# Performance work log

Hardware: AMD Instinct MI355X
Metric: run time of the kernel (lower is better)

The kernel has to match this reference:

```python
import jax, jax.numpy as jnp
import numpy as np

BETA = 0.25
DECAY = 0.99
USAGE_DECAY = 0.99
EPS = 1e-5
RESET_THRESHOLD = 100.0


def _sqdist(x, e):
    # squared euclidean distances [N, K]; argmin identical to cdist argmin
    x2 = jnp.sum(x * x, axis=1, keepdims=True)           # [N,1]
    e2 = jnp.sum(e * e, axis=1)[None, :]                 # [1,K]
    return x2 - 2.0 * (x @ e.T) + e2


def setup_inputs() -> dict:
    key = jax.random.key(0)
    ks = jax.random.split(key, 7)
    N, K, D = 32768, 4096, 256
    return {
        "x": jax.random.normal(ks[0], (N, D), jnp.float32),
        "embedding": jax.random.normal(ks[1], (K, D), jnp.float32) * (1.0 / K),
        "ema_cluster_size": jax.random.uniform(ks[2], (K,), jnp.float32),
        "ema_w": jax.random.normal(ks[3], (K, D), jnp.float32) * (1.0 / K),
        "codebook_usage": jax.random.uniform(ks[4], (K,), jnp.float32),
        "steps_since_used": jax.random.randint(ks[5], (K,), 0, 200, jnp.int32),
        "random_indices": jax.random.randint(ks[6], (K,), 0, N, jnp.int32),
    }


def reference(x, embedding, ema_cluster_size, ema_w, codebook_usage,
              steps_since_used, random_indices):
    N, D = x.shape
    K = embedding.shape[0]

    # --- nearest-code lookup ---
    d2 = _sqdist(x, embedding)                 # [N,K]
    indices = jnp.argmin(d2, axis=1)           # [N]
    q = jnp.take(embedding, indices, axis=0)   # [N,D]
    quantized = x + jax.lax.stop_gradient(q - x)

    commitment_loss = jnp.mean((x - jax.lax.stop_gradient(quantized)) ** 2)
    loss = BETA * commitment_loss

    # --- EMA codebook update (encodings.sum(0) and encodings.T @ x as segment sums) ---
    counts = jax.ops.segment_sum(jnp.ones((N,), x.dtype), indices, num_segments=K)
    dw = jax.ops.segment_sum(x, indices, num_segments=K)        # [K,D]
    new_cs = ema_cluster_size * DECAY + (1.0 - DECAY) * counts
    new_ema_w = ema_w * DECAY + (1.0 - DECAY) * dw
    n = jnp.sum(new_cs)
    cluster_size = (new_cs + EPS) / (n + K * EPS) * n
    new_embedding = new_ema_w / cluster_size[:, None]
    new_usage = codebook_usage * USAGE_DECAY + (1.0 - USAGE_DECAY) * counts

    # --- dead-code reset (uses the EMA-updated codebook, as in the original) ---
    idx2 = jnp.argmin(_sqdist(x, new_embedding), axis=1)
    used = jax.ops.segment_sum(jnp.ones((N,), x.dtype), idx2, num_segments=K) > 0
    steps = jnp.where(used, 0.0, steps_since_used.astype(x.dtype) + 1.0)
    dead = steps > RESET_THRESHOLD
    replacement = jnp.take(x, random_indices, axis=0)           # [K,D]
    new_embedding = jnp.where(dead[:, None], replacement, new_embedding)
    steps = jnp.where(dead, 0.0, steps)

    usage_rate = jnp.mean((new_usage > 0).astype(x.dtype))

    return (quantized, indices, loss, new_embedding, new_cs, new_ema_w,
            new_usage, steps, usage_rate)
```

## Files before the change

### kernel.cpp

```cpp
#include <hip/hip_runtime.h>
#include <math.h>

typedef float vf4 __attribute__((ext_vector_type(4)));
typedef _Float16 f16;
typedef _Float16 f16x8 __attribute__((ext_vector_type(8)));
typedef _Float16 f16x4 __attribute__((ext_vector_type(4)));
typedef float f32x4 __attribute__((ext_vector_type(4)));

static constexpr int Ncnt = 32768;
static constexpr int Kcb  = 4096;
static constexpr int Dim  = 256;

static constexpr float EPSf  = 1e-5f;
static constexpr float KEPSf = (float)(4096.0 * 1e-5);

static constexpr size_t OQ  = 0;
static constexpr size_t OI  = (size_t)Ncnt * Dim;
static constexpr size_t OL  = OI + Ncnt;
static constexpr size_t OE  = OL + 1;
static constexpr size_t OCS = OE + (size_t)Kcb * Dim;
static constexpr size_t OW  = OCS + Kcb;
static constexpr size_t OU  = OW + (size_t)Kcb * Dim;
static constexpr size_t OS  = OU + Kcb;
static constexpr size_t OR  = OS + Kcb;

#define GLD16(gp, lp)                                                   \
  __builtin_amdgcn_global_load_lds(                                     \
      (const __attribute__((address_space(1))) void*)(gp),              \
      (__attribute__((address_space(3))) void*)(lp), 16, 0, 0)

__device__ __forceinline__ float np_sq256(const float* __restrict__ p) {
  float tot[2];
  #pragma unroll
  for (int h = 0; h < 2; ++h) {
    const float* a = p + h * 128;
    float r[8];
    #pragma unroll
    for (int j = 0; j < 8; ++j) r[j] = __fmul_rn(a[j], a[j]);
    for (int i = 8; i < 128; i += 8)
      #pragma unroll
      for (int j = 0; j < 8; ++j) r[j] = __fadd_rn(r[j], __fmul_rn(a[i + j], a[i + j]));
    tot[h] = __fadd_rn(__fadd_rn(__fadd_rn(r[0], r[1]), __fadd_rn(r[2], r[3])),
                       __fadd_rn(__fadd_rn(r[4], r[5]), __fadd_rn(r[6], r[7])));
  }
  return __fadd_rn(tot[0], tot[1]);
}

__global__ void rowsq_np(const float* __restrict__ E, float* __restrict__ e2, int rows) {
  const int k = blockIdx.x * 256 + threadIdx.x;
  if (k < rows) e2[k] = np_sq256(E + (size_t)k * Dim);
}

__global__ void split_rows(const float* __restrict__ src, f16* __restrict__ dst,
                           const float scale, const int rows)
{
  const int i   = blockIdx.x * 256 + threadIdx.x;
  const int row = i >> 6;
  const int d0  = (i & 63) * 4;
  if (row >= rows) return;
  const vf4 v = *(const vf4*)(src + (size_t)row * 256 + d0);
  f16x4 hi, lo;
  #pragma unroll
  for (int j = 0; j < 4; ++j) {
    const float t = __fmul_rn(v[j], scale);
    const f16 h   = (f16)t;
    const float r = __fsub_rn(t, (float)h);
    hi[j] = h;
    lo[j] = (f16)r;
  }
  *(f16x4*)(dst + (size_t)row * 512 + d0)       = hi;
  *(f16x4*)(dst + (size_t)row * 512 + 256 + d0) = lo;
}

__global__ __launch_bounds__(256, 2) void mfma_argmin(
    const f16* __restrict__ Xs, const f16* __restrict__ Es,
    const float* __restrict__ e2, const float two_scale,
    int* __restrict__ cand)
{
  __shared__ __align__(16) f16 As[2][128 * 32];
  __shared__ __align__(16) f16 Bs[2][128 * 32];

  const int tid  = threadIdx.x;
  const int bid  = blockIdx.x;
  const int row0 = (bid >> 3) * 128;
  const int cg   = bid & 7;
  const int colbase = cg * 512;

  const int l  = tid & 63;
  const int wv = tid >> 6;
  const int wr = wv >> 1;
  const int wc = wv & 1;
  const int lc = l & 15;
  const int kc = l >> 4;

  const int srow = wv * 32 + (l >> 2);
  const int chs  = (l & 3) ^ ((l >> 3) & 3);

  const f16* aB0 = Xs + (size_t)(row0 + srow) * 512 + chs * 8;
  const f16* aB1 = aB0 + 16 * 512;

  const int ks = (kc ^ ((lc >> 1) & 3)) * 8;

  const float nts = -two_scale;

  float t1[16], t2[16];
  int   i1[16], i2[16];
  #pragma unroll
  for (int s = 0; s < 16; ++s) {
    t1[s] = INFINITY; t2[s] = INFINITY; i1[s] = 0x7fffffff; i2[s] = 0x7fffffff;
  }

  #pragma unroll 1
  for (int ct = 0; ct < 4; ++ct) {
    const f16* bB0 = Es + (size_t)(colbase + ct * 128 + srow) * 512 + chs * 8;
    const f16* bB1 = bB0 + 16 * 512;

    f32x4 acc[4][4];
    #pragma unroll
    for (int i = 0; i < 4; ++i)
      #pragma unroll
      for (int j = 0; j < 4; ++j)
        acc[i][j] = (f32x4){0.0f, 0.0f, 0.0f, 0.0f};

    GLD16(aB0, &As[0][wv * 1024]); GLD16(aB1, &As[0][wv * 1024 + 512]);
    GLD16(bB0, &Bs[0][wv * 1024]); GLD16(bB1, &Bs[0][wv * 1024 + 512]);
    __syncthreads();

    #pragma unroll
    for (int st = 0; st < 24; ++st) {
      const int cur = st & 1;
      const int nxt = cur ^ 1;

      if (st + 1 < 24) {
        const int sn = st + 1;
        const int aO = ((sn >> 3) == 1 ? 256 : 0) + (sn & 7) * 32;
        const int bO = ((sn >> 3) == 2 ? 256 : 0) + (sn & 7) * 32;
        GLD16(aB0 + aO, &As[nxt][wv * 1024]);
        GLD16(aB1 + aO, &As[nxt][wv * 1024 + 512]);
        GLD16(bB0 + bO, &Bs[nxt][wv * 1024]);
        GLD16(bB1 + bO, &Bs[nxt][wv * 1024 + 512]);
      }

      f16x8 af[4], bf[4];
      #pragma unroll
      for (int f = 0; f < 4; ++f) {
        af[f] = *(const f16x8*)(&As[cur][(wr * 64 + f * 16 + lc) * 32 + ks]);
        bf[f] = *(const f16x8*)(&Bs[cur][(wc * 64 + f * 16 + lc) * 32 + ks]);
      }

      #pragma unroll
      for (int fm = 0; fm < 4; ++fm)
        #pragma unroll
        for (int fn = 0; fn < 4; ++fn)
          acc[fm][fn] = __builtin_amdgcn_mfma_f32_16x16x32_f16(
              af[fm], bf[fn], acc[fm][fn], 0, 0, 0);

      __syncthreads();
    }

    float e2v[4];
    #pragma unroll
    for (int fn = 0; fn < 4; ++fn)
      e2v[fn] = e2[colbase + ct * 128 + wc * 64 + fn * 16 + lc];

    #pragma unroll
    for (int fm = 0; fm < 4; ++fm) {
      #pragma unroll
      for (int j = 0; j < 4; ++j) {
        const int s = fm * 4 + j;
        #pragma unroll
        for (int fn = 0; fn < 4; ++fn) {
          const int col = colbase + ct * 128 + wc * 64 + fn * 16 + lc;
          const float t = fmaf(nts, acc[fm][fn][j], e2v[fn]);
          if (t < t1[s]) {
            t2[s] = t1[s]; i2[s] = i1[s]; t1[s] = t; i1[s] = col;
          } else if (t < t2[s]) {
            t2[s] = t; i2[s] = col;
          }
        }
      }
    }
  }

  #pragma unroll
  for (int s = 0; s < 16; ++s) {
    #pragma unroll
    for (int m = 1; m < 16; m <<= 1) {
      const float p1 = __shfl_xor(t1[s], m);
      const float p2 = __shfl_xor(t2[s], m);
      const int   q1 = __shfl_xor(i1[s], m);
      const int   q2 = __shfl_xor(i2[s], m);
      const bool pl = (p1 < t1[s]) || (p1 == t1[s] && q1 < i1[s]);
      float n1, n2; int m1, m2;
      if (pl) {
        n1 = p1; m1 = q1;
        const bool sl = (t1[s] < p2) || (t1[s] == p2 && i1[s] < q2);
        n2 = sl ? t1[s] : p2; m2 = sl ? i1[s] : q2;
      } else {
        n1 = t1[s]; m1 = i1[s];
        const bool sl = (p1 < t2[s]) || (p1 == t2[s] && q1 < i2[s]);
        n2 = sl ? p1 : t2[s]; m2 = sl ? q1 : i2[s];
      }
      t1[s] = n1; i1[s] = m1; t2[s] = n2; i2[s] = m2;
    }
  }

  if (lc == 0) {
    #pragma unroll
    for (int fm = 0; fm < 4; ++fm)
      #pragma unroll
      for (int j = 0; j < 4; ++j) {
        const int s    = fm * 4 + j;
        const int rloc = wr * 64 + fm * 16 + kc * 4 + j;
        const size_t base = ((size_t)(row0 + rloc) * 8 + cg) * 4 + wc * 2;
        cand[base]     = i1[s];
        cand[base + 1] = i2[s];
      }
  }
}

__global__ void recheck(const float* __restrict__ X, const float* __restrict__ x2g,
                        const float* __restrict__ Eref, const float* __restrict__ e2ref,
                        const int* __restrict__ cand, int* __restrict__ idxo)
{
  __shared__ float Xl[8][256];
  const int tid  = threadIdx.x;
  const int rg   = tid >> 5;
  const int lr   = tid & 31;
  const int row0 = blockIdx.x * 8;
  const int row  = row0 + rg;

  {
    const float* xp = X + (size_t)row * 256 + lr * 8;
    *(vf4*)(&Xl[rg][lr * 8])     = *(const vf4*)xp;
    *(vf4*)(&Xl[rg][lr * 8 + 4]) = *(const vf4*)(xp + 4);
  }
  __syncthreads();

  int k = cand[(size_t)row * 32 + lr];

  float acc = 0.0f;
  const float* ep = Eref + (size_t)k * 256;
  for (int d4 = 0; d4 < 64; ++d4) {
    const vf4 xv = *(const vf4*)(&Xl[rg][d4 * 4]);
    const vf4 ev = *(const vf4*)(ep + d4 * 4);
    acc = fmaf(xv[0], ev[0], acc);
    acc = fmaf(xv[1], ev[1], acc);
    acc = fmaf(xv[2], ev[2], acc);
    acc = fmaf(xv[3], ev[3], acc);
  }
  float s = __fadd_rn(__fsub_rn(x2g[row], __fmul_rn(2.0f, acc)), e2ref[k]);

  #pragma unroll
  for (int m = 1; m < 32; m <<= 1) {
    const float os = __shfl_xor(s, m);
    const int   ok = __shfl_xor(k, m);
    if (os < s || (os == s && ok < k)) { s = os; k = ok; }
  }
  if (lr == 0) idxo[row] = k;
}

__global__ void stats_cd(const float* __restrict__ X, const float* __restrict__ E,
                         const int* __restrict__ idx, float* __restrict__ counts,
                         float* __restrict__ dw, double* __restrict__ loss_acc)
{
  __shared__ double part[4];
  const int tid  = threadIdx.x;
  const int lane = tid & 63, w = tid >> 6;
  const int row  = blockIdx.x * 4 + w;
  const int k    = idx[row];
  const vf4 xv = ((const vf4*)X)[(size_t)row * 64 + lane];
  const vf4 qv = ((const vf4*)E)[(size_t)k * 64 + lane];
  const float d0 = xv[0]-qv[0], d1 = xv[1]-qv[1], d2 = xv[2]-qv[2], d3 = xv[3]-qv[3];
  double ps = (double)(d0*d0 + d1*d1 + d2*d2 + d3*d3);
  #pragma unroll
  for (int o = 32; o; o >>= 1) ps += __shfl_down(ps, o);
  #pragma unroll
  for (int j = 0; j < 4; ++j)
    atomicAdd(dw + (size_t)k * Dim + lane * 4 + j, xv[j]);
  if (lane == 0) {
    part[w] = ps;
    atomicAdd(counts + k, 1.0f);
  }
  __syncthreads();
  if (tid == 0) atomicAdd(loss_acc, part[0] + part[1] + part[2] + part[3]);
}

__global__ void gather_q(const float* __restrict__ E, const int* __restrict__ idx,
                         float* __restrict__ out)
{
  const int tid  = threadIdx.x;
  const int lane = tid & 63, w = tid >> 6;
  const int row  = blockIdx.x * 4 + w;
  const int k    = idx[row];
  ((vf4*)out)[(size_t)row * 64 + lane] = ((const vf4*)E)[(size_t)k * 64 + lane];
  if (lane == 0) out[OI + row] = (float)k;
}

__global__ void cs_usage(const float* __restrict__ ecs, const float* __restrict__ usage,
                         const float* __restrict__ counts, float* __restrict__ out,
                         int* __restrict__ pos_cnt)
{
  __shared__ int si[256];
  const int tid = threadIdx.x;
  const int k   = blockIdx.x * 256 + tid;
  const float cnt = counts[k];
  const float ncs = __fadd_rn(__fmul_rn(ecs[k], 0.99f), __fmul_rn(0.01f, cnt));
  out[OCS + k] = ncs;
  const float nus = __fadd_rn(__fmul_rn(usage[k], 0.99f), __fmul_rn(0.01f, cnt));
  out[OU + k] = nus;
  si[tid] = (nus > 0.0f) ? 1 : 0;
  __syncthreads();
  for (int s = 128; s; s >>= 1) {
    if (tid < s) si[tid] += si[tid + s];
    __syncthreads();
  }
  if (tid == 0) atomicAdd(pos_cnt, si[0]);
}

__global__ void n_np_kernel(const float* __restrict__ ncs, float* __restrict__ nf) {
  __shared__ float leaf[32];
  const int t = threadIdx.x;
  if (t < 32) {
    const float* a = ncs + t * 128;
    float r[8];
    #pragma unroll
    for (int j = 0; j < 8; ++j) r[j] = a[j];
    for (int i = 8; i < 128; i += 8)
      #pragma unroll
      for (int j = 0; j < 8; ++j) r[j] = __fadd_rn(r[j], a[i + j]);
    leaf[t] = __fadd_rn(__fadd_rn(__fadd_rn(r[0], r[1]), __fadd_rn(r[2], r[3])),
                        __fadd_rn(__fadd_rn(r[4], r[5]), __fadd_rn(r[6], r[7])));
  }
  __syncthreads();
  if (t == 0) {
    float v[32];
    #pragma unroll
    for (int i = 0; i < 32; ++i) v[i] = leaf[i];
    for (int n = 32; n > 1; n >>= 1)
      for (int i = 0; i < (n >> 1); ++i) v[i] = __fadd_rn(v[2 * i], v[2 * i + 1]);
    *nf = v[0];
  }
}

__global__ void emb_pre(const float* __restrict__ emaw, float* __restrict__ out,
                        const float* __restrict__ nf)
{
  const int k = blockIdx.x;
  const int d = threadIdx.x;
  const size_t o = (size_t)k * Dim + d;
  const float dwv = out[OW + o];
  const float w = __fadd_rn(__fmul_rn(emaw[o], 0.99f), __fmul_rn(0.01f, dwv));
  out[OW + o] = w;
  const float nv  = *nf;
  const float ncs = out[OCS + k];
  const float cs  = __fmul_rn(__fdiv_rn(__fadd_rn(ncs, EPSf), __fadd_rn(nv, KEPSf)), nv);
  out[OE + o] = __fdiv_rn(w, cs);
}

__global__ void used_scatter(const int* __restrict__ idx2, int* __restrict__ used) {
  const int i = blockIdx.x * 256 + threadIdx.x;
  used[idx2[i]] = 1;
}

__global__ void finalize_k(const float* __restrict__ X, const int* __restrict__ used,
                           const int* __restrict__ steps_in, const int* __restrict__ rnd,
                           float* __restrict__ out)
{
  const int k = blockIdx.x, d = threadIdx.x;
  const int u = used[k];
  const float st = u ? 0.0f : (float)steps_in[k] + 1.0f;
  const bool dead = st > 100.0f;
  if (dead) out[OE + (size_t)k * Dim + d] = X[(size_t)rnd[k] * Dim + d];
  if (d == 0) out[OS + k] = dead ? 0.0f : st;
}

__global__ void write_scalars(const double* __restrict__ loss_acc,
                              const int* __restrict__ pos_cnt, float* __restrict__ out)
{
  if (threadIdx.x == 0) {
    out[OL] = 0.25f * (float)(*loss_acc / (double)((size_t)Ncnt * Dim));
    out[OR] = (float)(*pos_cnt) / (float)Kcb;
  }
}

extern "C" void kernel_launch(void* const* d_in, const int* in_sizes, int n_in,
                              void* d_out, int out_size, void* d_ws, size_t ws_size,
                              hipStream_t stream)
{
  const float* X     = (const float*)d_in[0];
  const float* E     = (const float*)d_in[1];
  const float* ECS   = (const float*)d_in[2];
  const float* EMAW  = (const float*)d_in[3];
  const float* USAGE = (const float*)d_in[4];
  const int*   STEPS = (const int*)d_in[5];
  const int*   RND   = (const int*)d_in[6];
  float* out = (float*)d_out;

  float* wsf = (float*)d_ws;
  float*  counts   = wsf;
  int*    used     = (int*)(wsf + 4096);
  double* loss_acc = (double*)(wsf + 8192);
  float*  nf       = wsf + 8194;
  int*    pos_cnt  = (int*)(wsf + 8195);
  const size_t ZN  = 8200;
  float* x2g  = wsf + 8320;
  float* e2   = wsf + 41088;
  float* e2p  = wsf + 45184;
  int*   idx1 = (int*)(wsf + 49280);
  int*   idx2 = (int*)(wsf + 82048);
  f16*   Es   = (f16*)(wsf + 114816);
  int*   cand = (int*)(wsf + 1163392);
  f16*   Xsp  = (f16*)out;

  hipMemsetAsync(d_ws, 0, ZN * sizeof(float), stream);
  hipMemsetAsync(out + OW, 0, (size_t)Kcb * Dim * sizeof(float), stream);

  rowsq_np     <<<Ncnt / 256, 256, 0, stream>>>(X, x2g, Ncnt);
  rowsq_np     <<<Kcb / 256,  256, 0, stream>>>(E, e2, Kcb);
  split_rows   <<<Ncnt / 4,   256, 0, stream>>>(X, Xsp, 64.0f, Ncnt);
  split_rows   <<<Kcb / 4,    256, 0, stream>>>(E, Es, 16777216.0f, Kcb);
  mfma_argmin  <<<2048,       256, 0, stream>>>(Xsp, Es, e2, 0x1p-29f, cand);
  recheck      <<<Ncnt / 8,   256, 0, stream>>>(X, x2g, E, e2, cand, idx1);
  stats_cd     <<<Ncnt / 4,   256, 0, stream>>>(X, E, idx1, counts, out + OW, loss_acc);
  cs_usage     <<<Kcb / 256,  256, 0, stream>>>(ECS, USAGE, counts, out, pos_cnt);
  n_np_kernel  <<<1,          64,  0, stream>>>(out + OCS, nf);
  emb_pre      <<<Kcb,        256, 0, stream>>>(EMAW, out, nf);
  rowsq_np     <<<Kcb / 256,  256, 0, stream>>>(out + OE, e2p, Kcb);
  split_rows   <<<Kcb / 4,    256, 0, stream>>>(out + OE, Es, 256.0f, Kcb);
  mfma_argmin  <<<2048,       256, 0, stream>>>(Xsp, Es, e2p, 0x1p-13f, cand);
  recheck      <<<Ncnt / 8,   256, 0, stream>>>(X, x2g, out + OE, e2p, cand, idx2);
  used_scatter <<<Ncnt / 256, 256, 0, stream>>>(idx2, used);
  finalize_k   <<<Kcb,        256, 0, stream>>>(X, used, STEPS, RND, out);
  gather_q     <<<Ncnt / 4,   256, 0, stream>>>(E, idx1, out);
  write_scalars<<<1,          64,  0, stream>>>(loss_acc, pos_cnt, out);

  (void)in_sizes; (void)n_in; (void)out_size; (void)ws_size;
}
```

Before: 1.961 ms.

## Triple-buffer LDS tiles with depth-2 prefetch across codebook tiles in argmin GEMM

After: 1.858 ms. 5.2% less time.

```diff
diff --git a/kernel.cpp b/kernel.cpp
--- a/kernel.cpp
+++ b/kernel.cpp
@@ -72,13 +72,23 @@
   *(f16x4*)(dst + (size_t)row * 512 + 256 + d0) = lo;
 }
 
+#define AOF(s) ((((s) >> 3) == 1 ? 256 : 0) + ((s) & 7) * 32)
+#define BOF(s) ((((s) >> 3) == 2 ? 256 : 0) + ((s) & 7) * 32)
+#define STAGE4(aP0, aP1, bP0, bP1, bufi)                                \
+  do {                                                                  \
+    GLD16((aP0), &As[(bufi)][wv * 1024]);                               \
+    GLD16((aP1), &As[(bufi)][wv * 1024 + 512]);                         \
+    GLD16((bP0), &Bs[(bufi)][wv * 1024]);                               \
+    GLD16((bP1), &Bs[(bufi)][wv * 1024 + 512]);                         \
+  } while (0)
+
 __global__ __launch_bounds__(256, 2) void mfma_argmin(
     const f16* __restrict__ Xs, const f16* __restrict__ Es,
     const float* __restrict__ e2, const float two_scale,
     int* __restrict__ cand)
 {
-  __shared__ __align__(16) f16 As[2][128 * 32];
-  __shared__ __align__(16) f16 Bs[2][128 * 32];
+  __shared__ __align__(16) f16 As[3][128 * 32];
+  __shared__ __align__(16) f16 Bs[3][128 * 32];
 
   const int tid  = threadIdx.x;
   const int bid  = blockIdx.x;
@@ -98,6 +108,8 @@
 
   const f16* aB0 = Xs + (size_t)(row0 + srow) * 512 + chs * 8;
   const f16* aB1 = aB0 + 16 * 512;
+  const f16* bBase0 = Es + (size_t)(colbase + srow) * 512 + chs * 8;
+  const f16* bBase1 = bBase0 + 16 * 512;
 
   const int ks = (kc ^ ((lc >> 1) & 3)) * 8;
 
@@ -110,10 +122,13 @@
     t1[s] = INFINITY; t2[s] = INFINITY; i1[s] = 0x7fffffff; i2[s] = 0x7fffffff;
   }
 
+  STAGE4(aB0 + AOF(0), aB1 + AOF(0), bBase0 + BOF(0), bBase1 + BOF(0), 0);
+  STAGE4(aB0 + AOF(1), aB1 + AOF(1), bBase0 + BOF(1), bBase1 + BOF(1), 1);
+
   #pragma unroll 1
   for (int ct = 0; ct < 4; ++ct) {
-    const f16* bB0 = Es + (size_t)(colbase + ct * 128 + srow) * 512 + chs * 8;
-    const f16* bB1 = bB0 + 16 * 512;
+    const f16* bC0 = bBase0 + ct * 65536;
+    const f16* bC1 = bBase1 + ct * 65536;
 
     f32x4 acc[4][4];
     #pragma unroll
@@ -122,25 +137,14 @@
       for (int j = 0; j < 4; ++j)
         acc[i][j] = (f32x4){0.0f, 0.0f, 0.0f, 0.0f};
 
-    GLD16(aB0, &As[0][wv * 1024]); GLD16(aB1, &As[0][wv * 1024 + 512]);
-    GLD16(bB0, &Bs[0][wv * 1024]); GLD16(bB1, &Bs[0][wv * 1024 + 512]);
-    __syncthreads();
-
     #pragma unroll
     for (int st = 0; st < 24; ++st) {
-      const int cur = st & 1;
-      const int nxt = cur ^ 1;
-
-      if (st + 1 < 24) {
-        const int sn = st + 1;
-        const int aO = ((sn >> 3) == 1 ? 256 : 0) + (sn & 7) * 32;
-        const int bO = ((sn >> 3) == 2 ? 256 : 0) + (sn & 7) * 32;
-        GLD16(aB0 + aO, &As[nxt][wv * 1024]);
-        GLD16(aB1 + aO, &As[nxt][wv * 1024 + 512]);
-        GLD16(bB0 + bO, &Bs[nxt][wv * 1024]);
-        GLD16(bB1 + bO, &Bs[nxt][wv * 1024 + 512]);
-      }
-
+      if (st == 23) { asm volatile("s_waitcnt vmcnt(0)" ::: "memory"); }
+      else          { asm volatile("s_waitcnt vmcnt(4)" ::: "memory"); }
+      __builtin_amdgcn_s_barrier();
+      __builtin_amdgcn_sched_barrier(0);
+
+      const int cur = st % 3;
       f16x8 af[4], bf[4];
       #pragma unroll
       for (int f = 0; f < 4; ++f) {
@@ -148,14 +152,23 @@
         bf[f] = *(const f16x8*)(&Bs[cur][(wc * 64 + f * 16 + lc) * 32 + ks]);
       }
 
+      if (st + 2 < 24) {
+        STAGE4(aB0 + AOF(st + 2), aB1 + AOF(st + 2),
+               bC0 + BOF(st + 2), bC1 + BOF(st + 2), (st + 2) % 3);
+      } else if (ct < 3) {
+        STAGE4(aB0 + AOF(st - 22), aB1 + AOF(st - 22),
+               bC0 + 65536 + BOF(st - 22), bC1 + 65536 + BOF(st - 22),
+               (st + 2) % 3);
+      }
+
+      __builtin_amdgcn_s_setprio(1);
       #pragma unroll
       for (int fm = 0; fm < 4; ++fm)
         #pragma unroll
         for (int fn = 0; fn < 4; ++fn)
           acc[fm][fn] = __builtin_amdgcn_mfma_f32_16x16x32_f16(
               af[fm], bf[fn], acc[fm][fn], 0, 0, 0);
-
-      __syncthreads();
+      __builtin_amdgcn_s_setprio(0);
     }
 
     float e2v[4];
```
